# Kernel tuning notes

Measured on AMD Instinct MI355X. Metric: run time of the kernel, lower is better.

## Reference

```python
import jax, jax.numpy as jnp
import numpy as np

B, T = 48, 88200          # batch of 2 s clips at internal_sr=44100
N_EXC, N_LOOP = 6, 2      # exc_order+1, loop_order+1


def invert_lpc(y, A):
    """x[t] = y[t] + sum_{k=1..N} A[:, t, k-1] * y[t-k]  (zi = 0).
    y: (B,T), A: (B,T,N) -> (B,T). Vectorized time-varying FIR."""
    Bs, Ts = y.shape
    N = A.shape[2]
    yp = jnp.pad(y, ((0, 0), (N, 0)))  # N leading zeros = zero initial state
    # shifts[:, t, k-1] = y[t-k]
    shifts = jnp.stack([yp[:, N - k:N - k + Ts] for k in range(1, N + 1)], axis=2)
    return y + jnp.sum(A * shifts, axis=2)


def sample_wise_lpc(x, A):
    """Time-varying all-pole IIR: y[t] = x[t] - sum_{k=1..N} A[:, t, k-1]*y[t-k].
    Sequential recurrence over T via lax.scan. x: (B,T), A: (B,T,N)."""
    Bs, Ts = x.shape
    N = A.shape[2]

    def step(carry, inp):
        # carry: (B,N) = [y[t-1], ..., y[t-N]]
        xt, at = inp  # (B,), (B,N)
        yt = xt - jnp.sum(at * carry, axis=1)
        new_carry = jnp.concatenate([yt[:, None], carry[:, :-1]], axis=1)
        return new_carry, yt

    carry0 = jnp.zeros((Bs, N), x.dtype)
    _, ys = jax.lax.scan(step, carry0, (x.T, jnp.swapaxes(A, 0, 1)))
    return ys.T  # (B,T)


def setup_inputs() -> dict:
    key = jax.random.key(0)
    k1, k2, k3 = jax.random.split(key, 3)
    y = jax.random.normal(k1, (B, T), dtype=jnp.float32)
    # excitation (FIR-inverse) coefficients: mild, zero-centered
    A_exc = (jax.random.uniform(k2, (B, T, N_EXC), dtype=jnp.float32) - 0.5) * 0.2
    # loop (all-pole) coefficients kept small so the IIR recurrence is stable
    A_loop = (jax.random.uniform(k3, (B, T, N_LOOP), dtype=jnp.float32) - 0.5) * 0.5
    return {"y": y, "A_exc": A_exc, "A_loop": A_loop}


def reference(y, A_exc, A_loop):
    # Core DiffKS pipeline kernel: inverse LPC (feed-forward comb/loop inversion)
    # followed by the sample-wise recursive LPC resynthesis (Karplus-Strong loop).
    x = invert_lpc(y, A_exc)
    return sample_wise_lpc(x, A_loop)
```

## Files before the change

### kernel.cpp

```cpp
#include <hip/hip_runtime.h>


#define T_LEN 88200
#define B_N   48
#define SPL   8
#define OUT_W 480
#define WUP   32
#define NCH   184
#define WPB   8
#define NWAVES (B_N * NCH)

__device__ __forceinline__ float4 zero4() { return make_float4(0.f, 0.f, 0.f, 0.f); }

__device__ __forceinline__ float4 ld_guard(const float* p, int t) {
    if (t >= 0 && t + 3 < T_LEN) return *(const float4*)(p + t);
    return zero4();
}

__global__ __launch_bounds__(512, 4) void diffks_kernel(
    const float* __restrict__ y, const float* __restrict__ A_exc,
    const float* __restrict__ A_loop, float* __restrict__ out) {
    const int tid  = threadIdx.x;
    const int widx = tid >> 6;
    const int lane = tid & 63;
    const int w = blockIdx.x * WPB + widx;
    const int b = w / NCH;
    const int c = w - b * NCH;
    const int s  = c * OUT_W;
    const int w0 = s - WUP;
    const int t0 = w0 + SPL * lane;

    const float* yb  = y      + (size_t)b * T_LEN;
    const float* aeb = A_exc  + (size_t)b * T_LEN * 6;
    const float* alb = A_loop + (size_t)b * T_LEN * 2;
    float*       ob  = out    + (size_t)b * T_LEN;

    const bool valid = (t0 >= 0) && (t0 < T_LEN);
    float4 yv0, yv1, ae[12], al[4];
    if (valid) {
        yv0 = *(const float4*)(yb + t0);
        yv1 = *(const float4*)(yb + t0 + 4);
        const float4* pae = (const float4*)(aeb + (size_t)t0 * 6);
#pragma unroll
        for (int k = 0; k < 12; ++k) ae[k] = pae[k];
        const float4* pal = (const float4*)(alb + (size_t)t0 * 2);
#pragma unroll
        for (int k = 0; k < 4; ++k) al[k] = pal[k];
    } else {
        yv0 = yv1 = zero4();
#pragma unroll
        for (int k = 0; k < 12; ++k) ae[k] = zero4();
#pragma unroll
        for (int k = 0; k < 4; ++k) al[k] = zero4();
    }

    float4 pv0, pv1;
    pv0.x = __shfl_up(yv0.x, 1, 64); pv0.y = __shfl_up(yv0.y, 1, 64);
    pv0.z = __shfl_up(yv0.z, 1, 64); pv0.w = __shfl_up(yv0.w, 1, 64);
    pv1.x = __shfl_up(yv1.x, 1, 64); pv1.y = __shfl_up(yv1.y, 1, 64);
    pv1.z = __shfl_up(yv1.z, 1, 64); pv1.w = __shfl_up(yv1.w, 1, 64);
    if (lane == 0) {
        pv0 = ld_guard(yb, t0 - 8);
        pv1 = ld_guard(yb, t0 - 4);
    }

    float yw[16] = { pv0.x, pv0.y, pv0.z, pv0.w, pv1.x, pv1.y, pv1.z, pv1.w,
                     yv0.x, yv0.y, yv0.z, yv0.w, yv1.x, yv1.y, yv1.z, yv1.w };
    float aef[48] = {
        ae[0].x, ae[0].y, ae[0].z, ae[0].w, ae[1].x, ae[1].y, ae[1].z, ae[1].w,
        ae[2].x, ae[2].y, ae[2].z, ae[2].w, ae[3].x, ae[3].y, ae[3].z, ae[3].w,
        ae[4].x, ae[4].y, ae[4].z, ae[4].w, ae[5].x, ae[5].y, ae[5].z, ae[5].w,
        ae[6].x, ae[6].y, ae[6].z, ae[6].w, ae[7].x, ae[7].y, ae[7].z, ae[7].w,
        ae[8].x, ae[8].y, ae[8].z, ae[8].w, ae[9].x, ae[9].y, ae[9].z, ae[9].w,
        ae[10].x, ae[10].y, ae[10].z, ae[10].w, ae[11].x, ae[11].y, ae[11].z, ae[11].w };
    float alf[16] = { al[0].x, al[0].y, al[0].z, al[0].w,
                      al[1].x, al[1].y, al[1].z, al[1].w,
                      al[2].x, al[2].y, al[2].z, al[2].w,
                      al[3].x, al[3].y, al[3].z, al[3].w };

    float xs[SPL];
    float p00 = 1.f, p01 = 0.f, p10 = 0.f, p11 = 1.f, c0 = 0.f, c1 = 0.f;
#pragma unroll
    for (int j = 0; j < SPL; ++j) {
        float xv = yw[8 + j];
#pragma unroll
        for (int k = 1; k <= 6; ++k)
            xv = fmaf(aef[j * 6 + (k - 1)], yw[8 + j - k], xv);
        xs[j] = xv;
        const float a1 = alf[2 * j], a2 = alf[2 * j + 1];
        const float n00 = fmaf(-a1, p00, -a2 * p10);
        const float n01 = fmaf(-a1, p01, -a2 * p11);
        p10 = p00; p11 = p01; p00 = n00; p01 = n01;
        const float nc0 = fmaf(-a1, c0, fmaf(-a2, c1, xv));
        c1 = c0; c0 = nc0;
    }

#pragma unroll
    for (int d = 1; d <= 2; d <<= 1) {
        const float q00 = __shfl_up(p00, d, 64), q01 = __shfl_up(p01, d, 64);
        const float q10 = __shfl_up(p10, d, 64), q11 = __shfl_up(p11, d, 64);
        const float qc0 = __shfl_up(c0, d, 64),  qc1 = __shfl_up(c1, d, 64);
        if (lane >= d) {
            const float m00 = fmaf(p00, q00, p01 * q10);
            const float m01 = fmaf(p00, q01, p01 * q11);
            const float m10 = fmaf(p10, q00, p11 * q10);
            const float m11 = fmaf(p10, q01, p11 * q11);
            const float nc0 = fmaf(p00, qc0, fmaf(p01, qc1, c0));
            const float nc1 = fmaf(p10, qc0, fmaf(p11, qc1, c1));
            p00 = m00; p01 = m01; p10 = m10; p11 = m11; c0 = nc0; c1 = nc1;
        }
    }
    {
        const float qc0 = __shfl_up(c0, 4, 64), qc1 = __shfl_up(c1, 4, 64);
        if (lane >= 4) {
            const float nc0 = fmaf(p00, qc0, fmaf(p01, qc1, c0));
            const float nc1 = fmaf(p10, qc0, fmaf(p11, qc1, c1));
            c0 = nc0; c1 = nc1;
        }
    }

    float y1 = __shfl_up(c0, 1, 64);
    float y2 = __shfl_up(c1, 1, 64);
    if (lane == 0) { y1 = 0.f; y2 = 0.f; }
#pragma unroll
    for (int j = 0; j < SPL; ++j) {
        const float yt = fmaf(-alf[2 * j], y1, fmaf(-alf[2 * j + 1], y2, xs[j]));
        y2 = y1; y1 = yt;
        xs[j] = yt;
    }

    if (lane >= 4 && t0 < T_LEN) {
        *(float4*)(ob + t0)     = make_float4(xs[0], xs[1], xs[2], xs[3]);
        *(float4*)(ob + t0 + 4) = make_float4(xs[4], xs[5], xs[6], xs[7]);
    }
}

extern "C" void kernel_launch(void* const* d_in, const int* in_sizes, int n_in,
                              void* d_out, int out_size, void* d_ws, size_t ws_size,
                              hipStream_t stream) {
    const float* y      = (const float*)d_in[0];
    const float* A_exc  = (const float*)d_in[1];
    const float* A_loop = (const float*)d_in[2];
    float* out = (float*)d_out;

    const int grid = NWAVES / WPB;
    diffks_kernel<<<grid, 512, 0, stream>>>(y, A_exc, A_loop, out);
}
```

Before: 198.3 us.

## Persistent single-wave blocks with double-buffered async global-to-LDS coefficient prefetch

Replaces the one-chunk-per-wave launch with 1024 persistent 64-thread blocks, each looping over chunks. While one chunk is being computed, the A_exc/A_loop coefficients for the next chunk are fetched into a double-buffered LDS area using global_load_lds, with manual vmcnt waits. The aim is to hide coefficient load latency behind compute. In exchange it reduces the number of resident waves, relies on hand-counted s_waitcnt values that the compiler may not preserve, and has no barrier or LDS-read wait around buffer reuse.

After: 191.2 us. -3.5%, faster.

```diff
diff --git a/kernel.cpp b/kernel.cpp
--- a/kernel.cpp
+++ b/kernel.cpp
@@ -7,8 +7,10 @@
 #define OUT_W 480
 #define WUP   32
 #define NCH   184
-#define WPB   8
-#define NWAVES (B_N * NCH)
+#define NCHUNKS (B_N * NCH)
+#define NPW   1024
+#define AE_F  3072
+#define AL_F  1024
 
 __device__ __forceinline__ float4 zero4() { return make_float4(0.f, 0.f, 0.f, 0.f); }
 
@@ -17,121 +19,170 @@
     return zero4();
 }
 
-__global__ __launch_bounds__(512, 4) void diffks_kernel(
+__device__ __forceinline__ void gload_lds16(const float* g, float* l) {
+    __builtin_amdgcn_global_load_lds(
+        (const __attribute__((address_space(1))) unsigned int*)g,
+        (__attribute__((address_space(3))) unsigned int*)l, 16, 0, 0);
+}
+
+__global__ __launch_bounds__(64) void diffks_kernel(
     const float* __restrict__ y, const float* __restrict__ A_exc,
     const float* __restrict__ A_loop, float* __restrict__ out) {
-    const int tid  = threadIdx.x;
-    const int widx = tid >> 6;
-    const int lane = tid & 63;
-    const int w = blockIdx.x * WPB + widx;
-    const int b = w / NCH;
-    const int c = w - b * NCH;
-    const int s  = c * OUT_W;
-    const int w0 = s - WUP;
-    const int t0 = w0 + SPL * lane;
+    __shared__ float sae[2][AE_F];
+    __shared__ float sal[2][AL_F];
+    const int lane = threadIdx.x;
+    const int g    = blockIdx.x;
 
-    const float* yb  = y      + (size_t)b * T_LEN;
-    const float* aeb = A_exc  + (size_t)b * T_LEN * 6;
-    const float* alb = A_loop + (size_t)b * T_LEN * 2;
-    float*       ob  = out    + (size_t)b * T_LEN;
-
-    const bool valid = (t0 >= 0) && (t0 < T_LEN);
-    float4 yv0, yv1, ae[12], al[4];
-    if (valid) {
-        yv0 = *(const float4*)(yb + t0);
-        yv1 = *(const float4*)(yb + t0 + 4);
-        const float4* pae = (const float4*)(aeb + (size_t)t0 * 6);
+    if (g != 0) {
+        const int b = g / NCH, c = g - b * NCH;
+        const ptrdiff_t w0 = (ptrdiff_t)c * OUT_W - WUP;
+        const float* ga = A_exc + ((ptrdiff_t)b * T_LEN + w0) * 6 + lane * 4;
+        const float* gl = A_loop + ((ptrdiff_t)b * T_LEN + w0) * 2 + lane * 4;
 #pragma unroll
-        for (int k = 0; k < 12; ++k) ae[k] = pae[k];
-        const float4* pal = (const float4*)(alb + (size_t)t0 * 2);
+        for (int j = 0; j < 12; ++j) gload_lds16(ga + j * 256, &sae[0][j * 256]);
 #pragma unroll
-        for (int k = 0; k < 4; ++k) al[k] = pal[k];
-    } else {
-        yv0 = yv1 = zero4();
-#pragma unroll
-        for (int k = 0; k < 12; ++k) ae[k] = zero4();
-#pragma unroll
-        for (int k = 0; k < 4; ++k) al[k] = zero4();
+        for (int j = 0; j < 4; ++j)  gload_lds16(gl + j * 256, &sal[0][j * 256]);
     }
 
-    float4 pv0, pv1;
-    pv0.x = __shfl_up(yv0.x, 1, 64); pv0.y = __shfl_up(yv0.y, 1, 64);
-    pv0.z = __shfl_up(yv0.z, 1, 64); pv0.w = __shfl_up(yv0.w, 1, 64);
-    pv1.x = __shfl_up(yv1.x, 1, 64); pv1.y = __shfl_up(yv1.y, 1, 64);
-    pv1.z = __shfl_up(yv1.z, 1, 64); pv1.w = __shfl_up(yv1.w, 1, 64);
-    if (lane == 0) {
-        pv0 = ld_guard(yb, t0 - 8);
-        pv1 = ld_guard(yb, t0 - 4);
-    }
+    int s = 0;
+    for (int k = g; k < NCHUNKS; k += NPW, s ^= 1) {
+        const int b  = k / NCH, c = k - b * NCH;
+        const int w0 = c * OUT_W - WUP;
+        const int t0 = w0 + SPL * lane;
+        const float* yb = y   + (size_t)b * T_LEN;
+        float*       ob = out + (size_t)b * T_LEN;
 
-    float yw[16] = { pv0.x, pv0.y, pv0.z, pv0.w, pv1.x, pv1.y, pv1.z, pv1.w,
-                     yv0.x, yv0.y, yv0.z, yv0.w, yv1.x, yv1.y, yv1.z, yv1.w };
-    float aef[48] = {
-        ae[0].x, ae[0].y, ae[0].z, ae[0].w, ae[1].x, ae[1].y, ae[1].z, ae[1].w,
-        ae[2].x, ae[2].y, ae[2].z, ae[2].w, ae[3].x, ae[3].y, ae[3].z, ae[3].w,
-        ae[4].x, ae[4].y, ae[4].z, ae[4].w, ae[5].x, ae[5].y, ae[5].z, ae[5].w,
-        ae[6].x, ae[6].y, ae[6].z, ae[6].w, ae[7].x, ae[7].y, ae[7].z, ae[7].w,
-        ae[8].x, ae[8].y, ae[8].z, ae[8].w, ae[9].x, ae[9].y, ae[9].z, ae[9].w,
-        ae[10].x, ae[10].y, ae[10].z, ae[10].w, ae[11].x, ae[11].y, ae[11].z, ae[11].w };
-    float alf[16] = { al[0].x, al[0].y, al[0].z, al[0].w,
-                      al[1].x, al[1].y, al[1].z, al[1].w,
-                      al[2].x, al[2].y, al[2].z, al[2].w,
-                      al[3].x, al[3].y, al[3].z, al[3].w };
+        const bool valid = (t0 >= 0) && (t0 < T_LEN);
+        float4 yv0, yv1;
+        if (valid) {
+            yv0 = *(const float4*)(yb + t0);
+            yv1 = *(const float4*)(yb + t0 + 4);
+        } else { yv0 = yv1 = zero4(); }
+        float4 h0 = zero4(), h1 = zero4();
+        if (lane == 0) {
+            h0 = ld_guard(yb, t0 - 8);
+            h1 = ld_guard(yb, t0 - 4);
+        }
 
-    float xs[SPL];
-    float p00 = 1.f, p01 = 0.f, p10 = 0.f, p11 = 1.f, c0 = 0.f, c1 = 0.f;
+        const int  kn = k + NPW;
+        const bool next_int = (kn < NCHUNKS - 1);
+        if (next_int) {
+            const int bn = kn / NCH, cn = kn - bn * NCH;
+            const ptrdiff_t wn = (ptrdiff_t)cn * OUT_W - WUP;
+            const float* ga = A_exc + ((ptrdiff_t)bn * T_LEN + wn) * 6 + lane * 4;
+            const float* gl = A_loop + ((ptrdiff_t)bn * T_LEN + wn) * 2 + lane * 4;
+            float* la = &sae[s ^ 1][0];
+            float* ll = &sal[s ^ 1][0];
 #pragma unroll
-    for (int j = 0; j < SPL; ++j) {
-        float xv = yw[8 + j];
+            for (int j = 0; j < 12; ++j) gload_lds16(ga + j * 256, la + j * 256);
 #pragma unroll
-        for (int k = 1; k <= 6; ++k)
-            xv = fmaf(aef[j * 6 + (k - 1)], yw[8 + j - k], xv);
-        xs[j] = xv;
-        const float a1 = alf[2 * j], a2 = alf[2 * j + 1];
-        const float n00 = fmaf(-a1, p00, -a2 * p10);
-        const float n01 = fmaf(-a1, p01, -a2 * p11);
-        p10 = p00; p11 = p01; p00 = n00; p01 = n01;
-        const float nc0 = fmaf(-a1, c0, fmaf(-a2, c1, xv));
-        c1 = c0; c0 = nc0;
-    }
+            for (int j = 0; j < 4; ++j)  gload_lds16(gl + j * 256, ll + j * 256);
+        }
+
+        float4 ae[12], al4[4];
+        const bool cur_int = (k != 0) && (k != NCHUNKS - 1);
+        if (cur_int) {
+            if (next_int) asm volatile("s_waitcnt vmcnt(16)" ::: "memory");
+            else          asm volatile("s_waitcnt vmcnt(0)"  ::: "memory");
+            const float4* pa = (const float4*)&sae[s][48 * lane];
+            const float4* pl = (const float4*)&sal[s][16 * lane];
+#pragma unroll
+            for (int j = 0; j < 12; ++j) ae[j] = pa[j];
+#pragma unroll
+            for (int j = 0; j < 4; ++j)  al4[j] = pl[j];
+        } else {
+            if (valid) {
+                const float4* pa = (const float4*)(A_exc + ((size_t)b * T_LEN + t0) * 6);
+                const float4* pl = (const float4*)(A_loop + ((size_t)b * T_LEN + t0) * 2);
+#pragma unroll
+                for (int j = 0; j < 12; ++j) ae[j] = pa[j];
+#pragma unroll
+                for (int j = 0; j < 4; ++j)  al4[j] = pl[j];
+            } else {
+#pragma unroll
+                for (int j = 0; j < 12; ++j) ae[j] = zero4();
+#pragma unroll
+                for (int j = 0; j < 4; ++j)  al4[j] = zero4();
+            }
+        }
+
+        float4 pv0, pv1;
+        pv0.x = __shfl_up(yv0.x, 1, 64); pv0.y = __shfl_up(yv0.y, 1, 64);
+        pv0.z = __shfl_up(yv0.z, 1, 64); pv0.w = __shfl_up(yv0.w, 1, 64);
+        pv1.x = __shfl_up(yv1.x, 1, 64); pv1.y = __shfl_up(yv1.y, 1, 64);
+        pv1.z = __shfl_up(yv1.z, 1, 64); pv1.w = __shfl_up(yv1.w, 1, 64);
+        if (lane == 0) { pv0 = h0; pv1 = h1; }
+
+        float yw[16] = { pv0.x, pv0.y, pv0.z, pv0.w, pv1.x, pv1.y, pv1.z, pv1.w,
+                         yv0.x, yv0.y, yv0.z, yv0.w, yv1.x, yv1.y, yv1.z, yv1.w };
+        float aef[48] = {
+            ae[0].x, ae[0].y, ae[0].z, ae[0].w, ae[1].x, ae[1].y, ae[1].z, ae[1].w,
+            ae[2].x, ae[2].y, ae[2].z, ae[2].w, ae[3].x, ae[3].y, ae[3].z, ae[3].w,
+            ae[4].x, ae[4].y, ae[4].z, ae[4].w, ae[5].x, ae[5].y, ae[5].z, ae[5].w,
+            ae[6].x, ae[6].y, ae[6].z, ae[6].w, ae[7].x, ae[7].y, ae[7].z, ae[7].w,
+            ae[8].x, ae[8].y, ae[8].z, ae[8].w, ae[9].x, ae[9].y, ae[9].z, ae[9].w,
+            ae[10].x, ae[10].y, ae[10].z, ae[10].w,
+            ae[11].x, ae[11].y, ae[11].z, ae[11].w };
+        float alf[16] = { al4[0].x, al4[0].y, al4[0].z, al4[0].w,
+                          al4[1].x, al4[1].y, al4[1].z, al4[1].w,
+                          al4[2].x, al4[2].y, al4[2].z, al4[2].w,
+                          al4[3].x, al4[3].y, al4[3].z, al4[3].w };
+
+        float xs[SPL];
+        float p00 = 1.f, p01 = 0.f, p10 = 0.f, p11 = 1.f, c0 = 0.f, c1 = 0.f;
+#pragma unroll
+        for (int j = 0; j < SPL; ++j) {
+            float xv = yw[8 + j];
+#pragma unroll
+            for (int kk = 1; kk <= 6; ++kk)
+                xv = fmaf(aef[j * 6 + (kk - 1)], yw[8 + j - kk], xv);
+            xs[j] = xv;
+            const float a1 = alf[2 * j], a2 = alf[2 * j + 1];
+            const float n00 = fmaf(-a1, p00, -a2 * p10);
+            const float n01 = fmaf(-a1, p01, -a2 * p11);
+            p10 = p00; p11 = p01; p00 = n00; p01 = n01;
+            const float nc0 = fmaf(-a1, c0, fmaf(-a2, c1, xv));
+            c1 = c0; c0 = nc0;
+        }
 
 #pragma unroll
-    for (int d = 1; d <= 2; d <<= 1) {
-        const float q00 = __shfl_up(p00, d, 64), q01 = __shfl_up(p01, d, 64);
-        const float q10 = __shfl_up(p10, d, 64), q11 = __shfl_up(p11, d, 64);
-        const float qc0 = __shfl_up(c0, d, 64),  qc1 = __shfl_up(c1, d, 64);
-        if (lane >= d) {
-            const float m00 = fmaf(p00, q00, p01 * q10);
-            const float m01 = fmaf(p00, q01, p01 * q11);
-            const float m10 = fmaf(p10, q00, p11 * q10);
-            const float m11 = fmaf(p10, q01, p11 * q11);
-            const float nc0 = fmaf(p00, qc0, fmaf(p01, qc1, c0));
-            const float nc1 = fmaf(p10, qc0, fmaf(p11, qc1, c1));
-            p00 = m00; p01 = m01; p10 = m10; p11 = m11; c0 = nc0; c1 = nc1;
+        for (int d = 1; d <= 2; d <<= 1) {
+            const float q00 = __shfl_up(p00, d, 64), q01 = __shfl_up(p01, d, 64);
+            const float q10 = __shfl_up(p10, d, 64), q11 = __shfl_up(p11, d, 64);
+            const float qc0 = __shfl_up(c0, d, 64),  qc1 = __shfl_up(c1, d, 64);
+            if (lane >= d) {
+                const float m00 = fmaf(p00, q00, p01 * q10);
+                const float m01 = fmaf(p00, q01, p01 * q11);
+                const float m10 = fmaf(p10, q00, p11 * q10);
+                const float m11 = fmaf(p10, q01, p11 * q11);
+                const float nc0 = fmaf(p00, qc0, fmaf(p01, qc1, c0));
+                const float nc1 = fmaf(p10, qc0, fmaf(p11, qc1, c1));
+                p00 = m00; p01 = m01; p10 = m10; p11 = m11; c0 = nc0; c1 = nc1;
+            }
         }
-    }
-    {
-        const float qc0 = __shfl_up(c0, 4, 64), qc1 = __shfl_up(c1, 4, 64);
-        if (lane >= 4) {
-            const float nc0 = fmaf(p00, qc0, fmaf(p01, qc1, c0));
-            const float nc1 = fmaf(p10, qc0, fmaf(p11, qc1, c1));
-            c0 = nc0; c1 = nc1;
+        {
+            const float qc0 = __shfl_up(c0, 4, 64), qc1 = __shfl_up(c1, 4, 64);
+            if (lane >= 4) {
+                const float nc0 = fmaf(p00, qc0, fmaf(p01, qc1, c0));
+                const float nc1 = fmaf(p10, qc0, fmaf(p11, qc1, c1));
+                c0 = nc0; c1 = nc1;
+            }
         }
-    }
 
-    float y1 = __shfl_up(c0, 1, 64);
-    float y2 = __shfl_up(c1, 1, 64);
-    if (lane == 0) { y1 = 0.f; y2 = 0.f; }
+        float y1 = __shfl_up(c0, 1, 64);
+        float y2 = __shfl_up(c1, 1, 64);
+        if (lane == 0) { y1 = 0.f; y2 = 0.f; }
 #pragma unroll
-    for (int j = 0; j < SPL; ++j) {
-        const float yt = fmaf(-alf[2 * j], y1, fmaf(-alf[2 * j + 1], y2, xs[j]));
-        y2 = y1; y1 = yt;
-        xs[j] = yt;
-    }
+        for (int j = 0; j < SPL; ++j) {
+            const float yt = fmaf(-alf[2 * j], y1, fmaf(-alf[2 * j + 1], y2, xs[j]));
+            y2 = y1; y1 = yt;
+            xs[j] = yt;
+        }
 
-    if (lane >= 4 && t0 < T_LEN) {
-        *(float4*)(ob + t0)     = make_float4(xs[0], xs[1], xs[2], xs[3]);
-        *(float4*)(ob + t0 + 4) = make_float4(xs[4], xs[5], xs[6], xs[7]);
+        if (lane >= 4 && t0 < T_LEN) {
+            *(float4*)(ob + t0)     = make_float4(xs[0], xs[1], xs[2], xs[3]);
+            *(float4*)(ob + t0 + 4) = make_float4(xs[4], xs[5], xs[6], xs[7]);
+        }
     }
 }
 
@@ -143,6 +194,5 @@
     const float* A_loop = (const float*)d_in[2];
     float* out = (float*)d_out;
 
-    const int grid = NWAVES / WPB;
-    diffks_kernel<<<grid, 512, 0, stream>>>(y, A_exc, A_loop, out);
+    diffks_kernel<<<NPW, 64, 0, stream>>>(y, A_exc, A_loop, out);
 }
```
